# Optimization experiments

Measured on AMD Instinct MI355X. Metric: run time of the kernel, lower is better.

Reference implementation:

```python
import jax, jax.numpy as jnp
import numpy as np

N_NODES = 20000
N_EDGES = 320000
VOCAB = 10000
D = 50          # F_in per tower (divide_input=False)
TOWERS = 5
F_OUT = 10      # out_channels // towers
N_LAYERS = 4
EPS_BN = 1e-5
EPS_STD = 1e-5


def setup_inputs() -> dict:
    key = jax.random.key(0)
    ks = jax.random.split(key, 24)
    rnd = lambda k, shape, s: (jax.random.normal(k, shape, jnp.float32) * s)
    inp = {
        "x": jax.random.randint(ks[0], (N_NODES,), 0, VOCAB, dtype=jnp.int32),
        "edge_index": jax.random.randint(ks[1], (2, N_EDGES), 0, N_NODES, dtype=jnp.int32),
        "edge_attr": jax.random.normal(ks[2], (N_EDGES, 4), jnp.float32),
        "batch": jnp.zeros((N_NODES,), jnp.int32),
        # parameters (stacked over the 4 conv layers)
        "emb": rnd(ks[3], (VOCAB, D), 1.0),
        "pre_W": rnd(ks[4], (N_LAYERS, TOWERS, D, 2 * D), 0.1),      # Linear(100,50) per tower
        "pre_b": rnd(ks[5], (N_LAYERS, TOWERS, D), 0.02),
        "post_W": rnd(ks[6], (N_LAYERS, TOWERS, F_OUT, 13 * D), 0.04),  # Linear(650,10) per tower
        "post_b": rnd(ks[7], (N_LAYERS, TOWERS, F_OUT), 0.02),
        "lin_W": rnd(ks[8], (N_LAYERS, D, D), 0.14),                 # Linear(50,50)
        "lin_b": rnd(ks[9], (N_LAYERS, D), 0.02),
        "bn_gamma": jnp.ones((N_LAYERS, D), jnp.float32),
        "bn_beta": jnp.zeros((N_LAYERS, D), jnp.float32),
        "mlp_W1": rnd(ks[10], (25, D), 0.14),
        "mlp_b1": rnd(ks[11], (25,), 0.02),
        "mlp_W2": rnd(ks[12], (1, 25), 0.2),
        "mlp_b2": rnd(ks[13], (1,), 0.02),
    }
    return inp


def _pna_conv(xh, src, dst, deg, avg_log, Wpre, bpre, Wpost, bpost, Wlin, blin):
    # xh: [N, D]. Pre-NN Linear(2D, D) per tower, applied to cat([x_i, x_j]).
    # Split the weight so we never materialize the [E, T, 2D] concat tensor.
    ai = jnp.einsum('nf,tgf->ntg', xh, Wpre[:, :, :D])   # x_i (target) part, [N,T,D]
    aj = jnp.einsum('nf,tgf->ntg', xh, Wpre[:, :, D:])   # x_j (source) part, [N,T,D]
    msg = ai[dst] + aj[src] + bpre[None]                 # [E,T,D]

    cnt = jnp.maximum(deg, 1.0)[:, None, None]           # clamped degree, [N,1,1]
    mean = jax.ops.segment_sum(msg, dst, N_NODES) / cnt
    mean_sq = jax.ops.segment_sum(msg * msg, dst, N_NODES) / cnt
    std = jnp.sqrt(jax.nn.relu(mean_sq - mean * mean) + EPS_STD)
    mn = jax.ops.segment_min(msg, dst, N_NODES)
    mx = jax.ops.segment_max(msg, dst, N_NODES)
    empty = (deg == 0)[:, None, None]                    # torch_scatter fills empties with 0
    mn = jnp.where(empty, 0.0, mn)
    mx = jnp.where(empty, 0.0, mx)

    agg = jnp.concatenate([mean, mn, mx, std], axis=-1)  # [N,T,4D] (aggregator order)
    sc = jnp.log(cnt + 1.0) / avg_log                    # amplification scaler
    out = jnp.concatenate([agg, agg * sc, agg / sc], axis=-1)   # identity/amp/atten -> [N,T,12D]

    xt = jnp.broadcast_to(xh[:, None, :], (xh.shape[0], TOWERS, D))
    h = jnp.concatenate([xt, out], axis=-1)              # [N,T,13D]
    y = jnp.einsum('ntf,tgf->ntg', h, Wpost) + bpost[None]  # post-NN per tower, [N,T,F_OUT]
    y = y.reshape(-1, TOWERS * F_OUT)                    # [N,50]
    return y @ Wlin.T + blin


def reference(x, edge_index, edge_attr, batch, emb, pre_W, pre_b, post_W, post_b,
              lin_W, lin_b, bn_gamma, bn_beta, mlp_W1, mlp_b1, mlp_W2, mlp_b2):
    src, dst = edge_index[0], edge_index[1]              # flow source_to_target
    deg = jax.ops.segment_sum(jnp.ones((src.shape[0],), jnp.float32), dst, N_NODES)
    avg_log = jnp.mean(jnp.log(deg + 1.0))               # PNA avg_deg['log'] from this graph

    h = emb[x]                                           # [N,D]
    for l in range(N_LAYERS):
        h = _pna_conv(h, src, dst, deg, avg_log, pre_W[l], pre_b[l],
                      post_W[l], post_b[l], lin_W[l], lin_b[l])
        mu = h.mean(axis=0)
        var = h.var(axis=0)                              # biased, as BatchNorm1d (train)
        h = jax.nn.relu(bn_gamma[l] * (h - mu) / jnp.sqrt(var + EPS_BN) + bn_beta[l])

    z = jax.nn.relu(h @ mlp_W1.T + mlp_b1)
    return jax.nn.sigmoid(z @ mlp_W2.T + mlp_b2)         # [N,1]
```

## Files before the change

### kernel.cpp

```cpp
#include <hip/hip_runtime.h>
#include <hip/hip_fp16.h>
#include <math.h>

#define NN 20000
#define NNP 20224
#define NGRP2 158
#define NE 320000
#define D 50
#define TOWERS 5
#define TD 250
#define ASTR 256
#define FOUT 10
#define EPS 1e-5f

__global__ void k_deg(const int* __restrict__ dst, int* __restrict__ deg) {
    int e = blockIdx.x * 256 + threadIdx.x;
    if (e < NE) atomicAdd(&deg[dst[e]], 1);
}

__global__ __launch_bounds__(256) void k_hist(const int* __restrict__ deg,
                                              int* __restrict__ hist) {
    __shared__ int lh[256];
    int tid = threadIdx.x;
    lh[tid] = 0;
    __syncthreads();
    int n = blockIdx.x * 256 + tid;
    if (n < NN) atomicAdd(&lh[min(deg[n], 255)], 1);
    __syncthreads();
    if (lh[tid] > 0) atomicAdd(&hist[tid], lh[tid]);
}

__global__ void k_binscan(const int* __restrict__ hist, int* __restrict__ binbase) {
    __shared__ int b[256];
    int tid = threadIdx.x;
    b[tid] = hist[tid];
    __syncthreads();
    for (int off = 1; off < 256; off <<= 1) {
        int t = (tid >= off) ? b[tid - off] : 0;
        __syncthreads();
        b[tid] += t;
        __syncthreads();
    }
    binbase[tid] = b[tid] - hist[tid];
}

__global__ __launch_bounds__(256) void k_scatter(
    const int* __restrict__ deg, const int* __restrict__ binbase,
    int* __restrict__ cursorb, int* __restrict__ perm,
    int* __restrict__ invp, int* __restrict__ deg_r) {
    __shared__ int lh[256];
    __shared__ int lbase[256];
    int tid = threadIdx.x;
    lh[tid] = 0;
    __syncthreads();
    int n = blockIdx.x * 256 + tid;
    int d = 0, slot = 0;
    bool ok = n < NN;
    if (ok) {
        d = min(deg[n], 255);
        slot = atomicAdd(&lh[d], 1);
    }
    __syncthreads();
    if (lh[tid] > 0) lbase[tid] = atomicAdd(&cursorb[tid], lh[tid]);
    __syncthreads();
    if (ok) {
        int r = binbase[d] + lbase[d] + slot;
        perm[r] = n;
        invp[n] = r;
        deg_r[r] = deg[n];
    }
}

__global__ void k_scan(const int* __restrict__ deg, int* __restrict__ offs) {
    __shared__ int buf[1024];
    __shared__ int carry;
    int tid = threadIdx.x;
    if (tid == 0) carry = 0;
    __syncthreads();
    for (int base = 0; base < NN; base += 1024) {
        int i = base + tid;
        int v = (i < NN) ? deg[i] : 0;
        buf[tid] = v;
        __syncthreads();
        for (int off = 1; off < 1024; off <<= 1) {
            int t = (tid >= off) ? buf[tid - off] : 0;
            __syncthreads();
            buf[tid] += t;
            __syncthreads();
        }
        int excl = carry + buf[tid] - v;
        if (i < NN) offs[i] = excl;
        __syncthreads();
        if (tid == 0) carry += buf[1023];
        __syncthreads();
    }
    if (tid == 0) offs[NN] = carry;
}

__global__ void k_csr(const int* __restrict__ src, const int* __restrict__ dst,
                      const int* __restrict__ offs, const int* __restrict__ invp,
                      int* __restrict__ cursor, int* __restrict__ csr_src) {
    int e = blockIdx.x * 256 + threadIdx.x;
    if (e < NE) {
        int rd = invp[dst[e]];
        int slot = atomicAdd(&cursor[rd], 1);
        csr_src[offs[rd] + slot] = invp[src[e]];
    }
}

__global__ void k_avglog(const int* __restrict__ deg, float* __restrict__ accum) {
    int n = blockIdx.x * 256 + threadIdx.x;
    float v = (n < NN) ? logf((float)deg[n] + 1.0f) : 0.0f;
    for (int o = 32; o > 0; o >>= 1) v += __shfl_down(v, o);
    __shared__ float wsum[4];
    int lane = threadIdx.x & 63, w = threadIdx.x >> 6;
    if (lane == 0) wsum[w] = v;
    __syncthreads();
    if (threadIdx.x == 0) atomicAdd(accum, wsum[0] + wsum[1] + wsum[2] + wsum[3]);
}

__global__ void k_emb(const int* __restrict__ x, const float* __restrict__ emb,
                      const int* __restrict__ perm, float* __restrict__ hT) {
    int idx = blockIdx.x * 256 + threadIdx.x;
    if (idx < D * NNP) {
        int c = idx / NNP, r = idx % NNP;
        hT[idx] = (r < NN) ? emb[x[perm[r]] * D + c] : 0.f;
    }
}

__global__ void k_wt(const float* __restrict__ postW, float* __restrict__ wT,
                     float* __restrict__ wxT) {
    int idx = blockIdx.x * 256 + threadIdx.x;
    const int WTN = 4 * TOWERS * 200 * 32;
    if (idx < WTN) {
        int l = idx / (TOWERS * 200 * 32);
        int r = idx % (TOWERS * 200 * 32);
        int t = r / (200 * 32); r %= 200 * 32;
        int j = r / 32, c = r % 32;
        float v = 0.f;
        if (c < 30) {
            int p = c / 10, g = c % 10;
            v = postW[l * 32500 + (t * FOUT + g) * 650 + 50 + p * 200 + j];
        }
        wT[idx] = v;
    } else if (idx < WTN + 4 * TOWERS * 50 * 16) {
        int k = idx - WTN;
        int l = k / (TOWERS * 50 * 16);
        int r = k % (TOWERS * 50 * 16);
        int t = r / (50 * 16); r %= 50 * 16;
        int j = r / 16, c = r % 16;
        float v = 0.f;
        if (c < 10) v = postW[l * 32500 + (t * FOUT + c) * 650 + j];
        wxT[k] = v;
    }
}

#define PRE_NT 16
__global__ __launch_bounds__(512) void k_pre(const float* __restrict__ hT,
                                             const float* __restrict__ preW,
                                             __half* __restrict__ aih,
                                             __half* __restrict__ ajh) {
    __shared__ float xl[PRE_NT * 52];
    int n0 = blockIdx.x * PRE_NT;
    int tid = threadIdx.x;
    for (int k = tid; k < PRE_NT * 52; k += 512) {
        int nl = k & 15, f = k >> 4;
        xl[nl * 52 + f] = (f < 50) ? hT[(size_t)f * NNP + n0 + nl] : 0.f;
    }
    __syncthreads();
    int isj = tid >> 8;
    int oo = tid & 255;
    __half* dstp = isj ? ajh : aih;
    if (oo < 250) {
        const float* w0 = preW + oo * 100 + isj * 50;
        float w[52];
#pragma unroll
        for (int f = 0; f < 50; ++f) w[f] = w0[f];
        w[50] = 0.f; w[51] = 0.f;
        for (int nl = 0; nl < PRE_NT; ++nl) {
            const float4* xv = (const float4*)&xl[nl * 52];
            float a0 = 0.f, a1 = 0.f, a2 = 0.f, a3 = 0.f;
#pragma unroll
            for (int j = 0; j < 12; j += 4) {
                float4 xa = xv[j], xb = xv[j + 1], xc = xv[j + 2], xd = xv[j + 3];
                a0 = fmaf(xa.x, w[4*j],   a0); a0 = fmaf(xa.y, w[4*j+1], a0);
                a0 = fmaf(xa.z, w[4*j+2], a0); a0 = fmaf(xa.w, w[4*j+3], a0);
                a1 = fmaf(xb.x, w[4*j+4], a1); a1 = fmaf(xb.y, w[4*j+5], a1);
                a1 = fmaf(xb.z, w[4*j+6], a1); a1 = fmaf(xb.w, w[4*j+7], a1);
                a2 = fmaf(xc.x, w[4*j+8], a2); a2 = fmaf(xc.y, w[4*j+9], a2);
                a2 = fmaf(xc.z, w[4*j+10], a2); a2 = fmaf(xc.w, w[4*j+11], a2);
                a3 = fmaf(xd.x, w[4*j+12], a3); a3 = fmaf(xd.y, w[4*j+13], a3);
                a3 = fmaf(xd.z, w[4*j+14], a3); a3 = fmaf(xd.w, w[4*j+15], a3);
            }
            float4 xe = xv[12];
            a0 = fmaf(xe.x, w[48], a0); a1 = fmaf(xe.y, w[49], a1);
            a2 = fmaf(xe.z, w[50], a2); a3 = fmaf(xe.w, w[51], a3);
            float a = (a0 + a1) + (a2 + a3);
            dstp[(size_t)(n0 + nl) * ASTR + oo] = __float2half(a);
        }
    } else {
        for (int nl = 0; nl < PRE_NT; ++nl)
            dstp[(size_t)(n0 + nl) * ASTR + oo] = __float2half(0.f);
    }
}

__global__ __launch_bounds__(512) void k_agg(
    const __half* __restrict__ aj, const int* __restrict__ offs,
    const int* __restrict__ csr_src, const __half* __restrict__ ai,
    const float* __restrict__ preB, __half* __restrict__ aggT) {
    int chunk = blockIdx.x & 3;
    int nb = (gridDim.x >> 2) - 1 - (blockIdx.x >> 2);
    int tid = threadIdx.x;
    int wave = tid >> 6, lane = tid & 63;
    int g = lane >> 3, q = lane & 7;
    int r = nb * 64 + wave * 8 + g;
    int coloff = chunk * 8 + q;
    bool ok = r < NN;
    int e0 = 0, dg = 0;
    if (ok) { e0 = offs[r]; dg = offs[r + 1] - e0; }
    int mdeg = dg;
#pragma unroll
    for (int o = 8; o < 64; o <<= 1) mdeg = min(mdeg, __shfl_xor(mdeg, o));

    const float4* ajv = (const float4*)aj;
    float s1[8], s2[8], mn[8], mx[8];
#pragma unroll
    for (int k = 0; k < 8; ++k) {
        s1[k] = 0.f; s2[k] = 0.f; mn[k] = INFINITY; mx[k] = -INFINITY;
    }

    int nblk = mdeg >> 2;
    int spref[4];
    if (nblk > 0) {
#pragma unroll
        for (int k = 0; k < 4; ++k) spref[k] = csr_src[e0 + k];
    }
    for (int b = 0; b < nblk; ++b) {
        int scur[4];
#pragma unroll
        for (int k = 0; k < 4; ++k) scur[k] = spref[k];
        int nxt = (b + 1 < nblk) ? (b + 1) * 4 : 0;
#pragma unroll
        for (int k = 0; k < 4; ++k) spref[k] = csr_src[e0 + nxt + k];
        float4 raw[4];
#pragma unroll
        for (int k = 0; k < 4; ++k)
            raw[k] = ajv[((unsigned)scur[k] << 5) + coloff];
#pragma unroll
        for (int k = 0; k < 4; ++k) {
            const __half2* hp = (const __half2*)&raw[k];
#pragma unroll
            for (int j = 0; j < 4; ++j) {
                float2 f = __half22float2(hp[j]);
                s1[2*j]   += f.x; s2[2*j]   = fmaf(f.x, f.x, s2[2*j]);
                mn[2*j]   = fminf(mn[2*j], f.x); mx[2*j]   = fmaxf(mx[2*j], f.x);
                s1[2*j+1] += f.y; s2[2*j+1] = fmaf(f.y, f.y, s2[2*j+1]);
                mn[2*j+1] = fminf(mn[2*j+1], f.y); mx[2*j+1] = fmaxf(mx[2*j+1], f.y);
            }
        }
    }
    int it = nblk << 2;
    for (; it < mdeg; ++it) {
        float4 raw = ajv[((unsigned)csr_src[e0 + it] << 5) + coloff];
        const __half2* hp = (const __half2*)&raw;
#pragma unroll
        for (int j = 0; j < 4; ++j) {
            float2 f = __half22float2(hp[j]);
            s1[2*j]   += f.x; s2[2*j]   = fmaf(f.x, f.x, s2[2*j]);
            mn[2*j]   = fminf(mn[2*j], f.x); mx[2*j]   = fmaxf(mx[2*j], f.x);
            s1[2*j+1] += f.y; s2[2*j+1] = fmaf(f.y, f.y, s2[2*j+1]);
            mn[2*j+1] = fminf(mn[2*j+1], f.y); mx[2*j+1] = fmaxf(mx[2*j+1], f.y);
        }
    }
    while (__any(it < dg)) {
        bool valid = it < dg;
        float4 raw = ajv[((unsigned)csr_src[valid ? e0 + it : e0] << 5) + coloff];
        const __half2* hp = (const __half2*)&raw;
#pragma unroll
        for (int j = 0; j < 4; ++j) {
            float2 f = __half22float2(hp[j]);
            float vx = valid ? f.x : 0.f, vy = valid ? f.y : 0.f;
            s1[2*j]   += vx; s2[2*j]   = fmaf(vx, vx, s2[2*j]);
            mn[2*j]   = fminf(mn[2*j], valid ? f.x : INFINITY);
            mx[2*j]   = fmaxf(mx[2*j], valid ? f.x : -INFINITY);
            s1[2*j+1] += vy; s2[2*j+1] = fmaf(vy, vy, s2[2*j+1]);
            mn[2*j+1] = fminf(mn[2*j+1], valid ? f.y : INFINITY);
            mx[2*j+1] = fmaxf(mx[2*j+1], valid ? f.y : -INFINITY);
        }
        ++it;
    }

    if (ok) {
        float inv = 1.0f / (float)max(dg, 1);
        float4 aihr = ((const float4*)ai)[(size_t)r * 32 + coloff];
        const __half2* ap = (const __half2*)&aihr;
        int f0 = coloff * 8;
#pragma unroll
        for (int j = 0; j < 4; ++j) {
            float2 av = __half22float2(ap[j]);
            float aval[2] = {av.x, av.y};
#pragma unroll
            for (int h = 0; h < 2; ++h) {
                int k = 2 * j + h;
                int f = f0 + k;
                if (f < TD) {
                    float m1 = s1[k] * inv;
                    float sd = sqrtf(fmaxf(s2[k] * inv - m1 * m1, 0.f) + EPS);
                    float mm, mnv, mxv;
                    if (dg > 0) {
                        float base = aval[h] + preB[f];
                        mm = m1 + base; mnv = mn[k] + base; mxv = mx[k] + base;
                    } else {
                        mm = 0.f; mnv = 0.f; mxv = 0.f; sd = sqrtf(EPS);
                    }
                    int t = f / 50, gg = f - t * 50;
                    __half* col = aggT + (size_t)(t * 200 + gg) * NNP + r;
                    col[0]                 = __float2half(mm);
                    col[(size_t)50 * NNP]  = __float2half(mnv);
                    col[(size_t)100 * NNP] = __float2half(mxv);
                    col[(size_t)150 * NNP] = __float2half(sd);
                }
            }
        }
    }
}

__global__ __launch_bounds__(256) void k_post(
    const float* __restrict__ hT, const __half* __restrict__ aggT,
    const int* __restrict__ offs,
    const float* __restrict__ wT,
    const float* __restrict__ wxT,
    const float* __restrict__ postB,
    const float* __restrict__ avg_accum, float* __restrict__ yT) {
    __shared__ float dp[128][33];
    int t = blockIdx.x / NGRP2;
    int grp = blockIdx.x - t * NGRP2;
    int tid = threadIdx.x;
    int hf = tid >> 7, ln = tid & 127;
    int hfu = __builtin_amdgcn_readfirstlane(hf);
    int n = grp * 128 + ln;

    float acc[30];
#pragma unroll
    for (int i = 0; i < 30; ++i) acc[i] = 0.f;
    const __half* aggcol = aggT + (size_t)(t * 200) * NNP + n;
    const float4* wv = (const float4*)(wT + t * 200 * 32);
    int j0 = hfu ? 80 : 0;
    int j1 = hfu ? 200 : 80;
#pragma unroll 4
    for (int j = j0; j < j1; ++j) {
        float a = __half2float(aggcol[(size_t)j * NNP]);
        float4 w0 = wv[j * 8 + 0], w1 = wv[j * 8 + 1], w2 = wv[j * 8 + 2],
               w3 = wv[j * 8 + 3], w4 = wv[j * 8 + 4], w5 = wv[j * 8 + 5],
               w6 = wv[j * 8 + 6], w7 = wv[j * 8 + 7];
        acc[0] = fmaf(a, w0.x, acc[0]);   acc[1] = fmaf(a, w0.y, acc[1]);
        acc[2] = fmaf(a, w0.z, acc[2]);   acc[3] = fmaf(a, w0.w, acc[3]);
        acc[4] = fmaf(a, w1.x, acc[4]);   acc[5] = fmaf(a, w1.y, acc[5]);
        acc[6] = fmaf(a, w1.z, acc[6]);   acc[7] = fmaf(a, w1.w, acc[7]);
        acc[8] = fmaf(a, w2.x, acc[8]);   acc[9] = fmaf(a, w2.y, acc[9]);
        acc[10] = fmaf(a, w2.z, acc[10]); acc[11] = fmaf(a, w2.w, acc[11]);
        acc[12] = fmaf(a, w3.x, acc[12]); acc[13] = fmaf(a, w3.y, acc[13]);
        acc[14] = fmaf(a, w3.z, acc[14]); acc[15] = fmaf(a, w3.w, acc[15]);
        acc[16] = fmaf(a, w4.x, acc[16]); acc[17] = fmaf(a, w4.y, acc[17]);
        acc[18] = fmaf(a, w4.z, acc[18]); acc[19] = fmaf(a, w4.w, acc[19]);
        acc[20] = fmaf(a, w5.x, acc[20]); acc[21] = fmaf(a, w5.y, acc[21]);
        acc[22] = fmaf(a, w5.z, acc[22]); acc[23] = fmaf(a, w5.w, acc[23]);
        acc[24] = fmaf(a, w6.x, acc[24]); acc[25] = fmaf(a, w6.y, acc[25]);
        acc[26] = fmaf(a, w6.z, acc[26]); acc[27] = fmaf(a, w6.w, acc[27]);
        acc[28] = fmaf(a, w7.x, acc[28]); acc[29] = fmaf(a, w7.y, acc[29]);
    }
    float xacc[10];
#pragma unroll
    for (int i = 0; i < 10; ++i) xacc[i] = 0.f;
    if (!hfu) {
        const float4* wxv = (const float4*)(wxT + t * 50 * 16);
#pragma unroll 2
        for (int j = 0; j < 50; ++j) {
            float a = hT[(size_t)j * NNP + n];
            float4 x0 = wxv[j * 4 + 0], x1 = wxv[j * 4 + 1], x2 = wxv[j * 4 + 2];
            xacc[0] = fmaf(a, x0.x, xacc[0]); xacc[1] = fmaf(a, x0.y, xacc[1]);
            xacc[2] = fmaf(a, x0.z, xacc[2]); xacc[3] = fmaf(a, x0.w, xacc[3]);
            xacc[4] = fmaf(a, x1.x, xacc[4]); xacc[5] = fmaf(a, x1.y, xacc[5]);
            xacc[6] = fmaf(a, x1.z, xacc[6]); xacc[7] = fmaf(a, x1.w, xacc[7]);
            xacc[8] = fmaf(a, x2.x, xacc[8]); xacc[9] = fmaf(a, x2.y, xacc[9]);
        }
    } else {
#pragma unroll
        for (int g = 0; g < 30; ++g) dp[ln][g] = acc[g];
    }
    __syncthreads();
    if (!hf && n < NN) {
        int dgn = offs[n + 1] - offs[n];
        float cnt = (float)max(dgn, 1);
        float sc = logf(cnt + 1.0f) / (avg_accum[0] * (1.0f / NN));
        float isc = 1.0f / sc;
#pragma unroll
        for (int g = 0; g < 10; ++g) {
            float a0 = acc[g] + dp[ln][g];
            float a1 = acc[10 + g] + dp[ln][10 + g];
            float a2 = acc[20 + g] + dp[ln][20 + g];
            yT[(size_t)(t * FOUT + g) * NNP + n] =
                postB[t * FOUT + g] + xacc[g] + a0 + sc * a1 + isc * a2;
        }
    }
}

__global__ __launch_bounds__(256) void k_lin(
    const float* __restrict__ yT, const float* __restrict__ linW,
    const float* __restrict__ linB, float* __restrict__ hrawT) {
    __shared__ float wl[2500];
    __shared__ float bl[50];
    int tid = threadIdx.x;
    int n = blockIdx.x * 256 + tid;
    for (int i = tid; i < 2500; i += 256) wl[i] = linW[i];
    if (tid < 50) bl[tid] = linB[tid];
    __syncthreads();
    float y[50];
#pragma unroll
    for (int q = 0; q < 50; ++q) y[q] = yT[(size_t)q * NNP + n];
    for (int c = 0; c < 50; ++c) {
        float a = bl[c];
        const float* w = wl + c * 50;
#pragma unroll
        for (int q = 0; q < 50; ++q) a = fmaf(w[q], y[q], a);
        hrawT[(size_t)c * NNP + n] = a;
    }
}

__global__ __launch_bounds__(256) void k_bnstats(const float* __restrict__ hrawT,
                                                 float* __restrict__ bn) {
    int c = blockIdx.x;
    int tid = threadIdx.x;
    const float* row = hrawT + (size_t)c * NNP;
    float s = 0.f, sq = 0.f;
    for (int n = tid; n < NN; n += 256) {
        float v = row[n];
        s += v; sq = fmaf(v, v, sq);
    }
    for (int o = 32; o > 0; o >>= 1) {
        s += __shfl_down(s, o);
        sq += __shfl_down(sq, o);
    }
    __shared__ float ws[4], wq[4];
    int lane = tid & 63, w = tid >> 6;
    if (lane == 0) { ws[w] = s; wq[w] = sq; }
    __syncthreads();
    if (tid == 0) {
        bn[c] = ws[0] + ws[1] + ws[2] + ws[3];
        bn[50 + c] = wq[0] + wq[1] + wq[2] + wq[3];
    }
}

__global__ void k_bnapply(const float* __restrict__ hrawT, const float* __restrict__ bn,
                          const float* __restrict__ gamma, const float* __restrict__ beta,
                          float* __restrict__ hT) {
    int idx = blockIdx.x * 256 + threadIdx.x;
    if (idx < D * NNP) {
        int c = idx / NNP, n = idx % NNP;
        float mean = bn[c] * (1.0f / NN);
        float var = bn[50 + c] * (1.0f / NN) - mean * mean;
        float v = gamma[c] * (hrawT[idx] - mean) * rsqrtf(var + EPS) + beta[c];
        hT[idx] = (n < NN) ? fmaxf(v, 0.f) : 0.f;
    }
}

__global__ void k_mlp(const float* __restrict__ hT, const int* __restrict__ perm,
                      const float* __restrict__ W1, const float* __restrict__ b1,
                      const float* __restrict__ W2, const float* __restrict__ b2,
                      float* __restrict__ out) {
    int n = blockIdx.x * 256 + threadIdx.x;
    if (n >= NN) return;
    float hv[50];
#pragma unroll
    for (int f = 0; f < 50; ++f) hv[f] = hT[(size_t)f * NNP + n];
    float s = b2[0];
    for (int o = 0; o < 25; ++o) {
        float a = b1[o];
        const float* w = W1 + o * 50;
#pragma unroll
        for (int f = 0; f < 50; ++f) a += w[f] * hv[f];
        s += W2[o] * fmaxf(a, 0.f);
    }
    out[perm[n]] = 1.0f / (1.0f + expf(-s));
}

extern "C" void kernel_launch(void* const* d_in, const int* in_sizes, int n_in,
                              void* d_out, int out_size, void* d_ws, size_t ws_size,
                              hipStream_t stream) {
    const int* x = (const int*)d_in[0];
    const int* ei = (const int*)d_in[1];
    const int* src = ei;
    const int* dst = ei + NE;
    const float* emb   = (const float*)d_in[4];
    const float* preW  = (const float*)d_in[5];
    const float* preB  = (const float*)d_in[6];
    const float* postW = (const float*)d_in[7];
    const float* postB = (const float*)d_in[8];
    const float* linW  = (const float*)d_in[9];
    const float* linB  = (const float*)d_in[10];
    const float* gamma = (const float*)d_in[11];
    const float* beta  = (const float*)d_in[12];
    const float* W1 = (const float*)d_in[13];
    const float* b1 = (const float*)d_in[14];
    const float* W2 = (const float*)d_in[15];
    const float* b2 = (const float*)d_in[16];
    float* outp = (float*)d_out;

    char* wsp = (char*)d_ws;
    size_t off = 0;
    auto alloc = [&](size_t bytes) {
        void* p = wsp + off;
        off = (off + bytes + 1023) & ~(size_t)1023;
        return p;
    };
    int* deg     = (int*)alloc(NN * 4);
    int* cursor  = (int*)alloc(NN * 4);
    int* offs    = (int*)alloc((NN + 1) * 4);
    int* csr     = (int*)alloc(NE * 4);
    int* perm    = (int*)alloc(NN * 4);
    int* invp    = (int*)alloc(NN * 4);
    int* deg_r   = (int*)alloc(NN * 4);
    int* hist    = (int*)alloc(256 * 4);
    int* binbase = (int*)alloc(256 * 4);
    int* cursorb = (int*)alloc(256 * 4);
    float* bn    = (float*)alloc(512);
    float* hT    = (float*)alloc((size_t)D * NNP * 4);
    float* hrawT = (float*)alloc((size_t)D * NNP * 4);
    float* yT    = (float*)alloc((size_t)D * NNP * 4);
    __half* aih  = (__half*)alloc((size_t)NN * ASTR * 2);
    __half* ajh  = (__half*)alloc((size_t)NN * ASTR * 2);
    float* wT    = (float*)alloc((size_t)4 * TOWERS * 200 * 32 * 4);
    float* wxT   = (float*)alloc((size_t)4 * TOWERS * 50 * 16 * 4);
    __half* aggT = (__half*)alloc((size_t)1000 * NNP * 2);
    (void)ws_size; (void)in_sizes; (void)n_in; (void)out_size;

    hipMemsetAsync(deg, 0, NN * 4, stream);
    hipMemsetAsync(cursor, 0, NN * 4, stream);
    hipMemsetAsync(hist, 0, 256 * 4, stream);
    hipMemsetAsync(cursorb, 0, 256 * 4, stream);
    hipMemsetAsync(bn, 0, 512, stream);

    k_deg<<<(NE + 255) / 256, 256, 0, stream>>>(dst, deg);
    k_hist<<<(NN + 255) / 256, 256, 0, stream>>>(deg, hist);
    k_binscan<<<1, 256, 0, stream>>>(hist, binbase);
    k_scatter<<<(NN + 255) / 256, 256, 0, stream>>>(deg, binbase, cursorb, perm, invp, deg_r);
    k_scan<<<1, 1024, 0, stream>>>(deg_r, offs);
    k_csr<<<(NE + 255) / 256, 256, 0, stream>>>(src, dst, offs, invp, cursor, csr);
    k_avglog<<<(NN + 255) / 256, 256, 0, stream>>>(deg, bn + 100);
    k_emb<<<(D * NNP + 255) / 256, 256, 0, stream>>>(x, emb, perm, hT);
    k_wt<<<(4 * TOWERS * 200 * 32 + 4 * TOWERS * 50 * 16 + 255) / 256, 256, 0, stream>>>(postW, wT, wxT);

    int aggblocks = 313 * 4;
    for (int l = 0; l < 4; ++l) {
        k_pre<<<NN / PRE_NT, 512, 0, stream>>>(hT, preW + l * TD * 100, aih, ajh);
        k_agg<<<aggblocks, 512, 0, stream>>>(ajh, offs, csr, aih, preB + l * TD, aggT);
        k_post<<<NGRP2 * TOWERS, 256, 0, stream>>>(hT, aggT, offs,
                                                   wT + l * TOWERS * 200 * 32,
                                                   wxT + l * TOWERS * 50 * 16,
                                                   postB + l * 50, bn + 100, yT);
        k_lin<<<NNP / 256, 256, 0, stream>>>(yT, linW + l * 2500, linB + l * 50, hrawT);
        k_bnstats<<<50, 256, 0, stream>>>(hrawT, bn);
        k_bnapply<<<(D * NNP + 255) / 256, 256, 0, stream>>>(hrawT, bn, gamma + l * 50,
                                                             beta + l * 50, hT);
    }
    k_mlp<<<(NN + 255) / 256, 256, 0, stream>>>(hT, perm, W1, b1, W2, b2, outp);
}
```

Measured before the change: 674.2 us.

## Derive CSR offsets and avg-log from degree histogram; split post GEMV four ways

```diff
diff --git a/kernel.cpp b/kernel.cpp
--- a/kernel.cpp
+++ b/kernel.cpp
@@ -30,18 +30,28 @@
     if (lh[tid] > 0) atomicAdd(&hist[tid], lh[tid]);
 }
 
-__global__ void k_binscan(const int* __restrict__ hist, int* __restrict__ binbase) {
+__global__ void k_binscan(const int* __restrict__ hist, int* __restrict__ binbase,
+                          int* __restrict__ ebase, float* __restrict__ avglog_out) {
     __shared__ int b[256];
-    int tid = threadIdx.x;
-    b[tid] = hist[tid];
+    __shared__ int eb[256];
+    __shared__ float lg[256];
+    int tid = threadIdx.x;
+    int h = hist[tid];
+    b[tid] = h;
+    eb[tid] = h * tid;
+    lg[tid] = (float)h * logf((float)tid + 1.0f);
     __syncthreads();
     for (int off = 1; off < 256; off <<= 1) {
-        int t = (tid >= off) ? b[tid - off] : 0;
+        int t1 = (tid >= off) ? b[tid - off] : 0;
+        int t2 = (tid >= off) ? eb[tid - off] : 0;
+        float t3 = (tid >= off) ? lg[tid - off] : 0.f;
         __syncthreads();
-        b[tid] += t;
+        b[tid] += t1; eb[tid] += t2; lg[tid] += t3;
         __syncthreads();
     }
-    binbase[tid] = b[tid] - hist[tid];
+    binbase[tid] = b[tid] - h;
+    ebase[tid] = eb[tid] - h * tid;
+    if (tid == 255) avglog_out[0] = lg[255];
 }
 
 __global__ __launch_bounds__(256) void k_scatter(
@@ -71,30 +81,15 @@
     }
 }
 
-__global__ void k_scan(const int* __restrict__ deg, int* __restrict__ offs) {
-    __shared__ int buf[1024];
-    __shared__ int carry;
-    int tid = threadIdx.x;
-    if (tid == 0) carry = 0;
-    __syncthreads();
-    for (int base = 0; base < NN; base += 1024) {
-        int i = base + tid;
-        int v = (i < NN) ? deg[i] : 0;
-        buf[tid] = v;
-        __syncthreads();
-        for (int off = 1; off < 1024; off <<= 1) {
-            int t = (tid >= off) ? buf[tid - off] : 0;
-            __syncthreads();
-            buf[tid] += t;
-            __syncthreads();
-        }
-        int excl = carry + buf[tid] - v;
-        if (i < NN) offs[i] = excl;
-        __syncthreads();
-        if (tid == 0) carry += buf[1023];
-        __syncthreads();
-    }
-    if (tid == 0) offs[NN] = carry;
+__global__ void k_offs(const int* __restrict__ deg_r, const int* __restrict__ binbase,
+                       const int* __restrict__ ebase, int* __restrict__ offs) {
+    int r = blockIdx.x * 256 + threadIdx.x;
+    if (r < NN) {
+        int d = deg_r[r];
+        int dc = min(d, 255);
+        offs[r] = ebase[dc] + (r - binbase[dc]) * d;
+    }
+    if (r == 0) offs[NN] = NE;
 }
 
 __global__ void k_csr(const int* __restrict__ src, const int* __restrict__ dst,
@@ -106,17 +101,6 @@
         int slot = atomicAdd(&cursor[rd], 1);
         csr_src[offs[rd] + slot] = invp[src[e]];
     }
-}
-
-__global__ void k_avglog(const int* __restrict__ deg, float* __restrict__ accum) {
-    int n = blockIdx.x * 256 + threadIdx.x;
-    float v = (n < NN) ? logf((float)deg[n] + 1.0f) : 0.0f;
-    for (int o = 32; o > 0; o >>= 1) v += __shfl_down(v, o);
-    __shared__ float wsum[4];
-    int lane = threadIdx.x & 63, w = threadIdx.x >> 6;
-    if (lane == 0) wsum[w] = v;
-    __syncthreads();
-    if (threadIdx.x == 0) atomicAdd(accum, wsum[0] + wsum[1] + wsum[2] + wsum[3]);
 }
 
 __global__ void k_emb(const int* __restrict__ x, const float* __restrict__ emb,
@@ -325,19 +309,19 @@
     }
 }
 
-__global__ __launch_bounds__(256) void k_post(
+__global__ __launch_bounds__(512) void k_post(
     const float* __restrict__ hT, const __half* __restrict__ aggT,
     const int* __restrict__ offs,
     const float* __restrict__ wT,
     const float* __restrict__ wxT,
     const float* __restrict__ postB,
     const float* __restrict__ avg_accum, float* __restrict__ yT) {
-    __shared__ float dp[128][33];
+    __shared__ float dp[3][128][33];
     int t = blockIdx.x / NGRP2;
     int grp = blockIdx.x - t * NGRP2;
     int tid = threadIdx.x;
-    int hf = tid >> 7, ln = tid & 127;
-    int hfu = __builtin_amdgcn_readfirstlane(hf);
+    int qd = tid >> 7, ln = tid & 127;
+    int qdu = __builtin_amdgcn_readfirstlane(qd);
     int n = grp * 128 + ln;
 
     float acc[30];
@@ -345,8 +329,8 @@
     for (int i = 0; i < 30; ++i) acc[i] = 0.f;
     const __half* aggcol = aggT + (size_t)(t * 200) * NNP + n;
     const float4* wv = (const float4*)(wT + t * 200 * 32);
-    int j0 = hfu ? 80 : 0;
-    int j1 = hfu ? 200 : 80;
+    int j0 = qdu * 50;
+    int j1 = j0 + 50;
 #pragma unroll 4
     for (int j = j0; j < j1; ++j) {
         float a = __half2float(aggcol[(size_t)j * NNP]);
@@ -372,7 +356,7 @@
     float xacc[10];
 #pragma unroll
     for (int i = 0; i < 10; ++i) xacc[i] = 0.f;
-    if (!hfu) {
+    if (qdu == 0) {
         const float4* wxv = (const float4*)(wxT + t * 50 * 16);
 #pragma unroll 2
         for (int j = 0; j < 50; ++j) {
@@ -386,19 +370,19 @@
         }
     } else {
 #pragma unroll
-        for (int g = 0; g < 30; ++g) dp[ln][g] = acc[g];
-    }
-    __syncthreads();
-    if (!hf && n < NN) {
+        for (int g = 0; g < 30; ++g) dp[qdu - 1][ln][g] = acc[g];
+    }
+    __syncthreads();
+    if (qd == 0 && n < NN) {
         int dgn = offs[n + 1] - offs[n];
         float cnt = (float)max(dgn, 1);
         float sc = logf(cnt + 1.0f) / (avg_accum[0] * (1.0f / NN));
         float isc = 1.0f / sc;
 #pragma unroll
         for (int g = 0; g < 10; ++g) {
-            float a0 = acc[g] + dp[ln][g];
-            float a1 = acc[10 + g] + dp[ln][10 + g];
-            float a2 = acc[20 + g] + dp[ln][20 + g];
+            float a0 = acc[g]      + dp[0][ln][g]      + dp[1][ln][g]      + dp[2][ln][g];
+            float a1 = acc[10 + g] + dp[0][ln][10 + g] + dp[1][ln][10 + g] + dp[2][ln][10 + g];
+            float a2 = acc[20 + g] + dp[0][ln][20 + g] + dp[1][ln][20 + g] + dp[2][ln][20 + g];
             yT[(size_t)(t * FOUT + g) * NNP + n] =
                 postB[t * FOUT + g] + xacc[g] + a0 + sc * a1 + isc * a2;
         }
@@ -522,6 +506,7 @@
     int* deg_r   = (int*)alloc(NN * 4);
     int* hist    = (int*)alloc(256 * 4);
     int* binbase = (int*)alloc(256 * 4);
+    int* ebase   = (int*)alloc(256 * 4);
     int* cursorb = (int*)alloc(256 * 4);
     float* bn    = (float*)alloc(512);
     float* hT    = (float*)alloc((size_t)D * NNP * 4);
@@ -542,11 +527,10 @@
 
     k_deg<<<(NE + 255) / 256, 256, 0, stream>>>(dst, deg);
     k_hist<<<(NN + 255) / 256, 256, 0, stream>>>(deg, hist);
-    k_binscan<<<1, 256, 0, stream>>>(hist, binbase);
+    k_binscan<<<1, 256, 0, stream>>>(hist, binbase, ebase, bn + 100);
     k_scatter<<<(NN + 255) / 256, 256, 0, stream>>>(deg, binbase, cursorb, perm, invp, deg_r);
-    k_scan<<<1, 1024, 0, stream>>>(deg_r, offs);
+    k_offs<<<(NN + 255) / 256, 256, 0, stream>>>(deg_r, binbase, ebase, offs);
     k_csr<<<(NE + 255) / 256, 256, 0, stream>>>(src, dst, offs, invp, cursor, csr);
-    k_avglog<<<(NN + 255) / 256, 256, 0, stream>>>(deg, bn + 100);
     k_emb<<<(D * NNP + 255) / 256, 256, 0, stream>>>(x, emb, perm, hT);
     k_wt<<<(4 * TOWERS * 200 * 32 + 4 * TOWERS * 50 * 16 + 255) / 256, 256, 0, stream>>>(postW, wT, wxT);
 
@@ -554,7 +538,7 @@
     for (int l = 0; l < 4; ++l) {
         k_pre<<<NN / PRE_NT, 512, 0, stream>>>(hT, preW + l * TD * 100, aih, ajh);
         k_agg<<<aggblocks, 512, 0, stream>>>(ajh, offs, csr, aih, preB + l * TD, aggT);
-        k_post<<<NGRP2 * TOWERS, 256, 0, stream>>>(hT, aggT, offs,
+        k_post<<<NGRP2 * TOWERS, 512, 0, stream>>>(hT, aggT, offs,
                                                    wT + l * TOWERS * 200 * 32,
                                                    wxT + l * TOWERS * 50 * 16,
                                                    postB + l * 50, bn + 100, yT);
```

Result: no change. 669.5 us (-0.7%).
